# Performance work log

Hardware: AMD Instinct MI355X
Metric: run time of the kernel (lower is better)

Reference implementation:

```python
import jax, jax.numpy as jnp
import numpy as np

N_FEATURES = 256
RAND_RANGE = 100.0


def _random_embed(x):
    """Deterministic pseudo-random embedding: each scalar in x seeds a counter-based
    RNG producing N_FEATURES uniforms in [0, RAND_RANGE). (JAX threefry replaces
    Python's Mersenne Twister; same structure: value-seeded deterministic uniforms.)"""
    flat = jax.lax.stop_gradient(x).reshape(-1)
    seeds = jax.lax.bitcast_convert_type(flat, jnp.uint32)  # value -> integer seed
    base = jax.random.key(42)
    keys = jax.vmap(lambda s: jax.random.fold_in(base, s))(seeds)
    emb = jax.vmap(lambda k: jax.random.uniform(k, (N_FEATURES,), minval=0.0, maxval=RAND_RANGE))(keys)
    return emb.reshape(x.shape + (N_FEATURES,))  # [B, S, F]


def setup_inputs() -> dict:
    key = jax.random.key(0)
    kx, kw, kb = jax.random.split(key, 3)
    x = jax.random.normal(kx, (256, 512), dtype=jnp.float32)
    W = jax.random.normal(kw, (N_FEATURES, N_FEATURES), dtype=jnp.float32) * 0.05
    b = jax.random.normal(kb, (N_FEATURES,), dtype=jnp.float32) * 0.05
    return {"x": x, "W": W, "b": b}


def reference(x, W, b):
    emb = _random_embed(x)                      # [B, S, F]
    out = jnp.einsum('bsf,gf->bsg', emb, W) + b  # nn.Linear: emb @ W.T + b
    return out
```

## Files before the change

kernel.cpp:

```cpp
#include <hip/hip_runtime.h>
#include <stdint.h>

#define F 256
#define R 64
#define THREADS 256
#define FPAD 264

typedef __attribute__((ext_vector_type(8))) short short8;
typedef __attribute__((ext_vector_type(4))) float floatx4;

__device__ __forceinline__ uint32_t rotl32(uint32_t x, int d) {
  return (x << d) | (x >> (32 - d));
}

__device__ __forceinline__ void tf2x32(uint32_t k0, uint32_t k1,
                                       uint32_t x0, uint32_t x1,
                                       uint32_t& o0, uint32_t& o1) {
  const uint32_t k2 = k0 ^ k1 ^ 0x1BD11BDAu;
  x0 += k0; x1 += k1;
#define TF_R4(a,b,c,d)                                    \
  x0 += x1; x1 = rotl32(x1,(a)); x1 ^= x0;                \
  x0 += x1; x1 = rotl32(x1,(b)); x1 ^= x0;                \
  x0 += x1; x1 = rotl32(x1,(c)); x1 ^= x0;                \
  x0 += x1; x1 = rotl32(x1,(d)); x1 ^= x0;
  TF_R4(13,15,26,6)
  x0 += k1; x1 += k2 + 1u;
  TF_R4(17,29,16,24)
  x0 += k2; x1 += k0 + 2u;
  TF_R4(13,15,26,6)
  x0 += k0; x1 += k1 + 3u;
  TF_R4(17,29,16,24)
  x0 += k1; x1 += k2 + 4u;
  TF_R4(13,15,26,6)
  x0 += k2; x1 += k0 + 5u;
#undef TF_R4
  o0 = x0; o1 = x1;
}

__device__ __forceinline__ float bits_to_unif(uint32_t bits) {
  uint32_t u = (bits >> 9) | 0x3F800000u;
  return fmaxf(0.0f, (__uint_as_float(u) - 1.0f) * 100.0f);
}

__device__ __forceinline__ uint16_t f2bf(float f) {
  uint32_t u = __float_as_uint(f);
  u += 0x7FFFu + ((u >> 16) & 1u);
  return (uint16_t)(u >> 16);
}

__global__ __launch_bounds__(THREADS) void FloatEmbedding_kernel(
    const float* __restrict__ x, const float* __restrict__ W,
    const float* __restrict__ bias, float* __restrict__ out) {
  __shared__ uint16_t semb[R][FPAD];
  __shared__ uint16_t sW[64][FPAD];
  __shared__ uint32_t skey[R][2];

  const int tid  = threadIdx.x;
  const int lane = tid & 63;
  const int wave = tid >> 6;
  const int qd   = lane >> 4;
  const int l16  = lane & 15;
  const size_t row0 = (size_t)blockIdx.x * R;

  if (tid < R) {
    uint32_t s = __float_as_uint(x[row0 + tid]);
    uint32_t o0, o1;
    tf2x32(0u, 42u, 0u, s, o0, o1);
    skey[tid][0] = o0; skey[tid][1] = o1;
  }
  __syncthreads();

  #pragma unroll 2
  for (int k = 0; k < R; ++k) {
    uint32_t k0 = skey[k][0], k1 = skey[k][1];
    uint32_t o0, o1;
    tf2x32(k0, k1, 0u, (uint32_t)tid, o0, o1);
    semb[k][tid] = f2bf(bits_to_unif(o0 ^ o1));
  }
  __syncthreads();

  for (int gt = 0; gt < 4; ++gt) {
    const float4* Wg4 = (const float4*)(W + (size_t)gt * 64 * F);
    #pragma unroll
    for (int c = 0; c < 16; ++c) {
      int q  = c * THREADS + tid;
      int g  = q >> 6;
      int fq = q & 63;
      float4 w4 = Wg4[g * 64 + fq];
      ushort4 b4 = make_ushort4(f2bf(w4.x), f2bf(w4.y), f2bf(w4.z), f2bf(w4.w));
      *(ushort4*)&sW[g][fq * 4] = b4;
    }
    __syncthreads();

    floatx4 acc[4];
    #pragma unroll
    for (int n = 0; n < 4; ++n) acc[n] = (floatx4){0.f, 0.f, 0.f, 0.f};

    const uint16_t* arow = &semb[wave * 16 + l16][qd * 8];
    #pragma unroll
    for (int kt = 0; kt < 8; ++kt) {
      short8 a = *(const short8*)(arow + kt * 32);
      #pragma unroll
      for (int n = 0; n < 4; ++n) {
        short8 b = *(const short8*)(&sW[n * 16 + l16][kt * 32 + qd * 8]);
        acc[n] = __builtin_amdgcn_mfma_f32_16x16x32_bf16(a, b, acc[n], 0, 0, 0);
      }
    }

    #pragma unroll
    for (int n = 0; n < 4; ++n) {
      int g = gt * 64 + n * 16 + l16;
      float bg = bias[g];
      #pragma unroll
      for (int reg = 0; reg < 4; ++reg) {
        size_t grow = row0 + (size_t)wave * 16 + qd * 4 + reg;
        out[grow * F + g] = acc[n][reg] + bg;
      }
    }
    __syncthreads();
  }
}

extern "C" void kernel_launch(void* const* d_in, const int* in_sizes, int n_in,
                              void* d_out, int out_size, void* d_ws, size_t ws_size,
                              hipStream_t stream) {
  const float* x = (const float*)d_in[0];
  const float* W = (const float*)d_in[1];
  const float* b = (const float*)d_in[2];
  float* out = (float*)d_out;
  const int nrows = in_sizes[0];
  const int blocks = nrows / R;
  hipLaunchKernelGGL(FloatEmbedding_kernel, dim3(blocks), dim3(THREADS), 0, stream,
                     x, W, b, out);
}
```

Before: 215.9 us.

## Pre-convert W to swizzled bf16 and stream chunks via global_load_lds

Adds a separate kernel that converts W to bf16 once per call in an XOR-swizzled layout in the workspace. The main kernel then loads 32-column chunks of W directly into LDS with global_load_lds instead of converting fp32 per block. It also hoists the A fragments into registers and sets launch bounds to 3 blocks per CU. The aim is less redundant conversion work, fewer LDS bank conflicts and lower LDS use for better occupancy. The cost is an extra kernel launch and twice as many chunk iterations, each with its own barriers.

```diff
diff --git a/kernel.cpp b/kernel.cpp
--- a/kernel.cpp
+++ b/kernel.cpp
@@ -4,7 +4,10 @@
 #define F 256
 #define R 64
 #define THREADS 256
-#define FPAD 264
+#define EPAD 264
+#define GCH 32
+#define NCH (F / GCH)
+#define SLOTS (GCH * F / 8)
 
 typedef __attribute__((ext_vector_type(8))) short short8;
 typedef __attribute__((ext_vector_type(4))) float floatx4;
@@ -48,11 +51,33 @@
   return (uint16_t)(u >> 16);
 }
 
-__global__ __launch_bounds__(THREADS) void FloatEmbedding_kernel(
-    const float* __restrict__ x, const float* __restrict__ W,
+__device__ __forceinline__ void gl_lds16(const void* gptr, void* lptr) {
+  __builtin_amdgcn_global_load_lds(
+      (const __attribute__((address_space(1))) uint32_t*)gptr,
+      (__attribute__((address_space(3))) uint32_t*)lptr, 16, 0, 0);
+}
+
+__global__ __launch_bounds__(256) void femb_conv(const float* __restrict__ W,
+                                                 uint16_t* __restrict__ ws) {
+  int s = blockIdx.x * 256 + threadIdx.x;
+  int row = s >> 5;
+  int c = s & 31;
+  int src_c = c ^ (row & 7);
+  const float4* src = (const float4*)(W + (size_t)row * F + src_c * 8);
+  float4 v0 = src[0], v1 = src[1];
+  short8 o;
+  o[0] = (short)f2bf(v0.x); o[1] = (short)f2bf(v0.y);
+  o[2] = (short)f2bf(v0.z); o[3] = (short)f2bf(v0.w);
+  o[4] = (short)f2bf(v1.x); o[5] = (short)f2bf(v1.y);
+  o[6] = (short)f2bf(v1.z); o[7] = (short)f2bf(v1.w);
+  *(short8*)(ws + (size_t)s * 8) = o;
+}
+
+__global__ __launch_bounds__(THREADS, 3) void femb_main(
+    const float* __restrict__ x, const uint16_t* __restrict__ Wbf,
     const float* __restrict__ bias, float* __restrict__ out) {
-  __shared__ uint16_t semb[R][FPAD];
-  __shared__ uint16_t sW[64][FPAD];
+  __shared__ uint16_t semb[R][EPAD];
+  __shared__ uint16_t sW[GCH * F];
   __shared__ uint32_t skey[R][2];
 
   const int tid  = threadIdx.x;
@@ -70,51 +95,50 @@
   }
   __syncthreads();
 
-  #pragma unroll 2
+  #pragma unroll 4
   for (int k = 0; k < R; ++k) {
-    uint32_t k0 = skey[k][0], k1 = skey[k][1];
     uint32_t o0, o1;
-    tf2x32(k0, k1, 0u, (uint32_t)tid, o0, o1);
+    tf2x32(skey[k][0], skey[k][1], 0u, (uint32_t)tid, o0, o1);
     semb[k][tid] = f2bf(bits_to_unif(o0 ^ o1));
   }
   __syncthreads();
 
-  for (int gt = 0; gt < 4; ++gt) {
-    const float4* Wg4 = (const float4*)(W + (size_t)gt * 64 * F);
+  const uint16_t* arow = &semb[wave * 16 + l16][qd * 8];
+  short8 afrag[8];
+  #pragma unroll
+  for (int kt = 0; kt < 8; ++kt) afrag[kt] = *(const short8*)(arow + kt * 32);
+
+  for (int gt = 0; gt < NCH; ++gt) {
+    const uint16_t* src = Wbf + (size_t)gt * SLOTS * 8;
     #pragma unroll
-    for (int c = 0; c < 16; ++c) {
-      int q  = c * THREADS + tid;
-      int g  = q >> 6;
-      int fq = q & 63;
-      float4 w4 = Wg4[g * 64 + fq];
-      ushort4 b4 = make_ushort4(f2bf(w4.x), f2bf(w4.y), f2bf(w4.z), f2bf(w4.w));
-      *(ushort4*)&sW[g][fq * 4] = b4;
+    for (int it = 0; it < SLOTS / THREADS; ++it) {
+      int sbase = it * THREADS + wave * 64;
+      gl_lds16(src + (size_t)(sbase + lane) * 8, &sW[(size_t)sbase * 8]);
     }
     __syncthreads();
 
-    floatx4 acc[4];
-    #pragma unroll
-    for (int n = 0; n < 4; ++n) acc[n] = (floatx4){0.f, 0.f, 0.f, 0.f};
-
-    const uint16_t* arow = &semb[wave * 16 + l16][qd * 8];
+    floatx4 acc[2];
+    acc[0] = (floatx4){0.f, 0.f, 0.f, 0.f};
+    acc[1] = (floatx4){0.f, 0.f, 0.f, 0.f};
     #pragma unroll
     for (int kt = 0; kt < 8; ++kt) {
-      short8 a = *(const short8*)(arow + kt * 32);
       #pragma unroll
-      for (int n = 0; n < 4; ++n) {
-        short8 b = *(const short8*)(&sW[n * 16 + l16][kt * 32 + qd * 8]);
-        acc[n] = __builtin_amdgcn_mfma_f32_16x16x32_bf16(a, b, acc[n], 0, 0, 0);
+      for (int n = 0; n < 2; ++n) {
+        int g = n * 16 + l16;
+        int slot = g * 32 + ((kt * 4 + qd) ^ (g & 7));
+        short8 b = *(const short8*)&sW[(size_t)slot * 8];
+        acc[n] = __builtin_amdgcn_mfma_f32_16x16x32_bf16(afrag[kt], b, acc[n], 0, 0, 0);
       }
     }
 
     #pragma unroll
-    for (int n = 0; n < 4; ++n) {
-      int g = gt * 64 + n * 16 + l16;
-      float bg = bias[g];
+    for (int n = 0; n < 2; ++n) {
+      int gg = gt * GCH + n * 16 + l16;
+      float bg = bias[gg];
       #pragma unroll
       for (int reg = 0; reg < 4; ++reg) {
         size_t grow = row0 + (size_t)wave * 16 + qd * 4 + reg;
-        out[grow * F + g] = acc[n][reg] + bg;
+        out[grow * F + gg] = acc[n][reg] + bg;
       }
     }
     __syncthreads();
@@ -128,8 +152,11 @@
   const float* W = (const float*)d_in[1];
   const float* b = (const float*)d_in[2];
   float* out = (float*)d_out;
+  uint16_t* wsbf = (uint16_t*)d_ws;
   const int nrows = in_sizes[0];
   const int blocks = nrows / R;
-  hipLaunchKernelGGL(FloatEmbedding_kernel, dim3(blocks), dim3(THREADS), 0, stream,
-                     x, W, b, out);
+
+  hipLaunchKernelGGL(femb_conv, dim3((F * F / 8) / 256), dim3(256), 0, stream, W, wsbf);
+  hipLaunchKernelGGL(femb_main, dim3(blocks), dim3(THREADS), 0, stream,
+                     x, wsbf, b, out);
 }
```

Result: faster. 198.9 us (-7.8%).
